# Optimization experiments

Hardware: AMD Instinct MI355X
Metric: run time of the kernel (lower is better)

The kernel has to match this reference:

```python
import jax, jax.numpy as jnp
import numpy as np

IOU_THRESHOLD = 0.5


def _make_boxes(key, n, canvas=800.0, min_size=8.0, max_size=160.0):
    k1, k2 = jax.random.split(key)
    cxy = jax.random.uniform(k1, (n, 2), dtype=jnp.float32) * canvas
    wh = min_size + jax.random.uniform(k2, (n, 2), dtype=jnp.float32) * (max_size - min_size)
    return jnp.concatenate([cxy - 0.5 * wh, cxy + 0.5 * wh], axis=1)  # [n,4] x1,y1,x2,y2


def setup_inputs() -> dict:
    key = jax.random.key(0)
    kp, kg, kl = jax.random.split(key, 3)
    N, M = 262144, 256
    proposals = _make_boxes(kp, N)
    gt_boxes = _make_boxes(kg, M)
    gt_labels = jax.random.randint(kl, (M,), 1, 21, dtype=jnp.int64)  # foreground classes 1..20
    return {"proposals": proposals, "gt_boxes": gt_boxes, "gt_labels": gt_labels}


def box_iou(a, b):
    # a: [N,4], b: [M,4] in x1,y1,x2,y2 -> [N,M]
    area_a = (a[:, 2] - a[:, 0]) * (a[:, 3] - a[:, 1])
    area_b = (b[:, 2] - b[:, 0]) * (b[:, 3] - b[:, 1])
    lt = jnp.maximum(a[:, None, :2], b[None, :, :2])
    rb = jnp.minimum(a[:, None, 2:], b[None, :, 2:])
    wh = jnp.clip(rb - lt, 0.0)
    inter = wh[..., 0] * wh[..., 1]
    union = area_a[:, None] + area_b[None, :] - inter
    return inter / union


def encode_boxes(props, gts):
    pw = props[:, 2] - props[:, 0]
    ph = props[:, 3] - props[:, 1]
    px = props[:, 0] + 0.5 * pw
    py = props[:, 1] + 0.5 * ph
    gw = gts[:, 2] - gts[:, 0]
    gh = gts[:, 3] - gts[:, 1]
    gx = gts[:, 0] + 0.5 * gw
    gy = gts[:, 1] + 0.5 * gh
    tx = (gx - px) / pw
    ty = (gy - py) / ph
    tw = jnp.log(gw / pw)
    th = jnp.log(gh / ph)
    return jnp.stack([tx, ty, tw, th], axis=1)


@jax.jit
def reference(proposals, gt_boxes, gt_labels):
    iou = box_iou(proposals, gt_boxes)            # [N,M] -- the memory-bound intermediate
    max_iou = jnp.max(iou, axis=1)                # [N]
    max_idx = jnp.argmax(iou, axis=1)             # [N]
    pos_mask = max_iou >= IOU_THRESHOLD
    roi_labels = jnp.where(pos_mask, gt_labels[max_idx], jnp.zeros_like(gt_labels[max_idx]))
    matched_gt = gt_boxes[max_idx]                # [N,4]
    deltas = encode_boxes(proposals, matched_gt)  # [N,4]
    roi_reg_targets = jnp.where(pos_mask[:, None], deltas, jnp.zeros_like(deltas))
    return roi_labels, roi_reg_targets
```

## Files before the change

kernel.cpp:

```cpp
#include <hip/hip_runtime.h>

#define M_GT 256

__global__ __launch_bounds__(256, 4) void roi_assign_kernel(
    const float4* __restrict__ proposals,
    const float4* __restrict__ gt_boxes,
    const int*    __restrict__ gt_labels,
    float*        __restrict__ out_labels,
    float4*       __restrict__ out_deltas,
    int N)
{
    __shared__ float4 s_box[M_GT];
    __shared__ float  s_area[M_GT];

    int tid = threadIdx.x;
    float4 g0 = gt_boxes[tid];
    s_box[tid]  = g0;
    s_area[tid] = (g0.z - g0.x) * (g0.w - g0.y);
    __syncthreads();

    int i = blockIdx.x * blockDim.x + tid;
    if (i >= N) return;

    float4 p = proposals[i];
    float areaA = (p.z - p.x) * (p.w - p.y);

    float biE = -1.f, buE = 1.f; int bxE = 0;
    float biO = -1.f, buO = 1.f; int bxO = 1;

    const float2* s_area2 = reinterpret_cast<const float2*>(s_area);

#pragma unroll 4
    for (int j = 0; j < M_GT; j += 2) {
        float4 gE = s_box[j];
        float4 gO = s_box[j + 1];
        float2 ar = s_area2[j >> 1];

        {
            float lx = fmaxf(p.x, gE.x), ly = fmaxf(p.y, gE.y);
            float rx = fminf(p.z, gE.z), ry = fminf(p.w, gE.w);
            float w = fmaxf(rx - lx, 0.f), h = fmaxf(ry - ly, 0.f);
            float inter = w * h;
            float uni = (areaA + ar.x) - inter;
            bool upd = (inter * buE) > (biE * uni);
            biE = upd ? inter : biE;
            buE = upd ? uni   : buE;
            bxE = upd ? j     : bxE;
        }
        {
            float lx = fmaxf(p.x, gO.x), ly = fmaxf(p.y, gO.y);
            float rx = fminf(p.z, gO.z), ry = fminf(p.w, gO.w);
            float w = fmaxf(rx - lx, 0.f), h = fmaxf(ry - ly, 0.f);
            float inter = w * h;
            float uni = (areaA + ar.y) - inter;
            bool upd = (inter * buO) > (biO * uni);
            biO = upd ? inter : biO;
            buO = upd ? uni   : buO;
            bxO = upd ? j + 1 : bxO;
        }
    }

    float ca = biO * buE, cb = biE * buO;
    bool takeO = (ca > cb) || ((ca == cb) && (bxO < bxE));
    float bi = takeO ? biO : biE;
    float bu = takeO ? buO : buE;
    int   bx = takeO ? bxO : bxE;

    float max_iou = bi / bu;
    bool pos = (max_iou >= 0.5f);

    out_labels[i] = pos ? (float)gt_labels[bx] : 0.0f;

    float4 g = s_box[bx];

    float pw = p.z - p.x;
    float ph = p.w - p.y;
    float px = p.x + 0.5f * pw;
    float py = p.y + 0.5f * ph;
    float gw = g.z - g.x;
    float gh = g.w - g.y;
    float gx = g.x + 0.5f * gw;
    float gy = g.y + 0.5f * gh;

    float tx = (gx - px) / pw;
    float ty = (gy - py) / ph;
    float tw = logf(gw / pw);
    float th = logf(gh / ph);

    float4 d;
    if (pos) { d.x = tx; d.y = ty; d.z = tw; d.w = th; }
    else     { d.x = 0.f; d.y = 0.f; d.z = 0.f; d.w = 0.f; }
    out_deltas[i] = d;
}

extern "C" void kernel_launch(void* const* d_in, const int* in_sizes, int n_in,
                              void* d_out, int out_size, void* d_ws, size_t ws_size,
                              hipStream_t stream) {
    const float4* proposals = (const float4*)d_in[0];
    const float4* gt_boxes  = (const float4*)d_in[1];
    const int*    gt_labels = (const int*)d_in[2];

    int N = in_sizes[0] / 4;

    float*  out_labels = (float*)d_out;
    float4* out_deltas = (float4*)((float*)d_out + N);

    dim3 block(256);
    dim3 grid((N + 255) / 256);
    roi_assign_kernel<<<grid, block, 0, stream>>>(
        proposals, gt_boxes, gt_labels, out_labels, out_deltas, N);
}
```

Measured before the change: 97.78 us.

## Split each proposal's GT scan across two threads and compare IoU via inter/sum

```diff
diff --git a/kernel.cpp b/kernel.cpp
--- a/kernel.cpp
+++ b/kernel.cpp
@@ -2,7 +2,7 @@
 
 #define M_GT 256
 
-__global__ __launch_bounds__(256, 4) void roi_assign_kernel(
+__global__ __launch_bounds__(256) void roi_assign_kernel(
     const float4* __restrict__ proposals,
     const float4* __restrict__ gt_boxes,
     const int*    __restrict__ gt_labels,
@@ -19,19 +19,23 @@
     s_area[tid] = (g0.z - g0.x) * (g0.w - g0.y);
     __syncthreads();
 
-    int i = blockIdx.x * blockDim.x + tid;
+    int p_local = tid >> 1;
+    int part    = tid & 1;
+    int i = blockIdx.x * 128 + p_local;
     if (i >= N) return;
 
     float4 p = proposals[i];
     float areaA = (p.z - p.x) * (p.w - p.y);
 
-    float biE = -1.f, buE = 1.f; int bxE = 0;
-    float biO = -1.f, buO = 1.f; int bxO = 1;
+    int jbase = part << 7;
+    float biE = -1.f, bSE = 1.f; int bxE = jbase;
+    float biO = -1.f, bSO = 1.f; int bxO = jbase + 1;
 
     const float2* s_area2 = reinterpret_cast<const float2*>(s_area);
 
-#pragma unroll 4
-    for (int j = 0; j < M_GT; j += 2) {
+#pragma unroll 8
+    for (int k = 0; k < 64; ++k) {
+        int j = jbase + (k << 1);
         float4 gE = s_box[j];
         float4 gO = s_box[j + 1];
         float2 ar = s_area2[j >> 1];
@@ -41,10 +45,10 @@
             float rx = fminf(p.z, gE.z), ry = fminf(p.w, gE.w);
             float w = fmaxf(rx - lx, 0.f), h = fmaxf(ry - ly, 0.f);
             float inter = w * h;
-            float uni = (areaA + ar.x) - inter;
-            bool upd = (inter * buE) > (biE * uni);
+            float S = areaA + ar.x;
+            bool upd = (inter * bSE) > (biE * S);
             biE = upd ? inter : biE;
-            buE = upd ? uni   : buE;
+            bSE = upd ? S     : bSE;
             bxE = upd ? j     : bxE;
         }
         {
@@ -52,45 +56,56 @@
             float rx = fminf(p.z, gO.z), ry = fminf(p.w, gO.w);
             float w = fmaxf(rx - lx, 0.f), h = fmaxf(ry - ly, 0.f);
             float inter = w * h;
-            float uni = (areaA + ar.y) - inter;
-            bool upd = (inter * buO) > (biO * uni);
+            float S = areaA + ar.y;
+            bool upd = (inter * bSO) > (biO * S);
             biO = upd ? inter : biO;
-            buO = upd ? uni   : buO;
+            bSO = upd ? S     : bSO;
             bxO = upd ? j + 1 : bxO;
         }
     }
 
-    float ca = biO * buE, cb = biE * buO;
+    float ca = biO * bSE, cb = biE * bSO;
     bool takeO = (ca > cb) || ((ca == cb) && (bxO < bxE));
     float bi = takeO ? biO : biE;
-    float bu = takeO ? buO : buE;
+    float bS = takeO ? bSO : bSE;
     int   bx = takeO ? bxO : bxE;
 
-    float max_iou = bi / bu;
-    bool pos = (max_iou >= 0.5f);
+    float o_bi = __shfl_xor(bi, 1);
+    float o_bS = __shfl_xor(bS, 1);
+    int   o_bx = __shfl_xor(bx, 1);
 
-    out_labels[i] = pos ? (float)gt_labels[bx] : 0.0f;
+    float b0i = part ? o_bi : bi,  b1i = part ? bi : o_bi;
+    float b0S = part ? o_bS : bS,  b1S = part ? bS : o_bS;
+    int   b0x = part ? o_bx : bx,  b1x = part ? bx : o_bx;
 
-    float4 g = s_box[bx];
+    bool take1 = (b1i * b0S) > (b0i * b1S);
+    float mI = take1 ? b1i : b0i;
+    float mS = take1 ? b1S : b0S;
+    int   mx = take1 ? b1x : b0x;
 
-    float pw = p.z - p.x;
-    float ph = p.w - p.y;
-    float px = p.x + 0.5f * pw;
-    float py = p.y + 0.5f * ph;
-    float gw = g.z - g.x;
-    float gh = g.w - g.y;
-    float gx = g.x + 0.5f * gw;
-    float gy = g.y + 0.5f * gh;
+    float uni = mS - mI;
+    float iou = mI / uni;
+    bool pos = (iou >= 0.5f);
 
-    float tx = (gx - px) / pw;
-    float ty = (gy - py) / ph;
-    float tw = logf(gw / pw);
-    float th = logf(gh / ph);
-
-    float4 d;
-    if (pos) { d.x = tx; d.y = ty; d.z = tw; d.w = th; }
-    else     { d.x = 0.f; d.y = 0.f; d.z = 0.f; d.w = 0.f; }
-    out_deltas[i] = d;
+    if (part == 0) {
+        out_labels[i] = pos ? (float)gt_labels[mx] : 0.0f;
+    } else {
+        float4 g = s_box[mx];
+        float pw = p.z - p.x, ph = p.w - p.y;
+        float px = p.x + 0.5f * pw, py = p.y + 0.5f * ph;
+        float gw = g.z - g.x, gh = g.w - g.y;
+        float gx = g.x + 0.5f * gw, gy = g.y + 0.5f * gh;
+        float4 d;
+        if (pos) {
+            d.x = (gx - px) / pw;
+            d.y = (gy - py) / ph;
+            d.z = logf(gw / pw);
+            d.w = logf(gh / ph);
+        } else {
+            d.x = 0.f; d.y = 0.f; d.z = 0.f; d.w = 0.f;
+        }
+        out_deltas[i] = d;
+    }
 }
 
 extern "C" void kernel_launch(void* const* d_in, const int* in_sizes, int n_in,
@@ -106,7 +121,7 @@
     float4* out_deltas = (float4*)((float*)d_out + N);
 
     dim3 block(256);
-    dim3 grid((N + 255) / 256);
+    dim3 grid((N + 127) / 128);
     roi_assign_kernel<<<grid, block, 0, stream>>>(
         proposals, gt_boxes, gt_labels, out_labels, out_deltas, N);
 }
```

Measured after the change: 94.51 us. 1.03x faster.
